# Kernel tuning notes

Hardware: AMD Instinct MI355X
Metric: run time of the kernel (lower is better)

## Reference

```python
import jax, jax.numpy as jnp
import numpy as np

NUM_HEADS = 8

def _qkv(t, W, b, H):
    # t: [B, L, C] -> q, k, v each [B, H, L, D]
    B, L, C = t.shape
    D = C // H
    qkv = (t @ W + b).reshape(B, L, 3, H, D)
    qkv = jnp.moveaxis(qkv, 2, 0)           # [3, B, L, H, D]
    qkv = jnp.swapaxes(qkv, 2, 3)           # [3, B, H, L, D]
    return qkv[0], qkv[1], qkv[2]

def _attend(q, k, v, scale):
    # q,k,v: [B, H, L, D] -> [B, L, C]
    B, H, L, D = q.shape
    scores = jnp.einsum('bhqd,bhkd->bhqk', q, k) * scale
    attn = jax.nn.softmax(scores, axis=-1)
    out = jnp.einsum('bhqk,bhkd->bhqd', attn, v)
    return jnp.swapaxes(out, 1, 2).reshape(B, L, H * D)

def setup_inputs() -> dict:
    key = jax.random.key(0)
    ks = jax.random.split(key, 7)
    B, N, C = 8, 2048, 512
    s_in = 1.0 / np.sqrt(C)
    return {
        'x': jax.random.normal(ks[0], (B, N, C), dtype=jnp.float32),
        'W_rgb_qkv': jax.random.normal(ks[1], (C, 3 * C), dtype=jnp.float32) * s_in,
        'b_rgb_qkv': jax.random.normal(ks[2], (3 * C,), dtype=jnp.float32) * 0.02,
        'W_depth_qkv': jax.random.normal(ks[3], (C, 3 * C), dtype=jnp.float32) * s_in,
        'b_depth_qkv': jax.random.normal(ks[4], (3 * C,), dtype=jnp.float32) * 0.02,
        'W_proj': jax.random.normal(ks[5], (C, C), dtype=jnp.float32) * s_in,
        'b_proj': jax.random.normal(ks[6], (C,), dtype=jnp.float32) * 0.02,
    }

def reference(x, W_rgb_qkv, b_rgb_qkv, W_depth_qkv, b_depth_qkv, W_proj, b_proj):
    B, N, C = x.shape
    H = NUM_HEADS
    D = C // H
    scale = D ** -0.5
    L = N // 2
    rgb, depth = x[:, :L], x[:, L:]
    rq, rk, rv = _qkv(rgb, W_rgb_qkv, b_rgb_qkv, H)
    dq, dk, dv = _qkv(depth, W_depth_qkv, b_depth_qkv, H)
    # rgb queries attend to depth K/V (named depth_v in torch code)
    depth_out = _attend(rq, dk, dv, scale)
    # depth queries attend to rgb K/V (named rgb_v in torch code)
    rgb_out = _attend(dq, rk, rv, scale)
    out = jnp.concatenate([rgb_out, depth_out], axis=1)  # [B, N, C]
    return out @ W_proj + b_proj
```

## Files before the change

### kernel.cpp

```cpp
#include <hip/hip_runtime.h>
#include <hip/hip_bf16.h>

typedef __attribute__((ext_vector_type(8))) short s16x8;
typedef __attribute__((ext_vector_type(4))) float f32x4;

__device__ __forceinline__ ushort f2bf(float f) {
  union { float f; unsigned int u; } c; c.f = f;
  unsigned int u = c.u + 0x7fffu + ((c.u >> 16) & 1u);
  return (ushort)(u >> 16);
}

__device__ __forceinline__ unsigned int pack2(float lo, float hi) {
  __hip_bfloat162 b2 = __float22bfloat162_rn(make_float2(lo, hi));
  union { __hip_bfloat162 b; unsigned int u; } c; c.b = b2;
  return c.u;
}

__device__ __forceinline__ s16x8 ld16(const ushort* p) {
  union { uint4 u; s16x8 s; } c;
  c.u = *reinterpret_cast<const uint4*>(p);
  return c.s;
}

__device__ __forceinline__ f32x4 mfma16(s16x8 a, s16x8 b, f32x4 c) {
  return __builtin_amdgcn_mfma_f32_16x16x32_bf16(a, b, c, 0, 0, 0);
}

__device__ __forceinline__ float exp2fast(float x) { return __builtin_amdgcn_exp2f(x); }

__device__ __forceinline__ void gld_lds16(const void* g, void* l) {
  __builtin_amdgcn_global_load_lds(
      (const __attribute__((address_space(1))) void*)g,
      (__attribute__((address_space(3))) void*)l, 16, 0, 0);
}


__global__ __launch_bounds__(256) void k_prep(
    const float* __restrict__ x, ushort* __restrict__ xb,
    const float* __restrict__ Wr, ushort* __restrict__ WtR,
    const float* __restrict__ Wd, ushort* __restrict__ WtD,
    const float* __restrict__ Wp, ushort* __restrict__ WtP) {
  __shared__ float tile[32][33];
  int b = blockIdx.x, t = threadIdx.x;
  if (b < 8192) {
    int i = (b * 256 + t) * 4;
    float4 v = *reinterpret_cast<const float4*>(x + i);
    ushort4 o;
    o.x = f2bf(v.x); o.y = f2bf(v.y); o.z = f2bf(v.z); o.w = f2bf(v.w);
    *reinterpret_cast<ushort4*>(xb + i) = o;
    return;
  }
  b -= 8192;
  const float* src; ushort* dst; int N;
  if (b < 768)      { src = Wr; dst = WtR; N = 1536; }
  else if (b < 1536){ b -= 768;  src = Wd; dst = WtD; N = 1536; }
  else              { b -= 1536; src = Wp; dst = WtP; N = 512; }
  int nb = N >> 5;
  int n0 = (b % nb) * 32, k0 = (b / nb) * 32;
  int tx = t & 31, ty = t >> 5;
#pragma unroll
  for (int i = 0; i < 32; i += 8)
    tile[ty + i][tx] = src[(k0 + ty + i) * N + (n0 + tx)];
  __syncthreads();
#pragma unroll
  for (int i = 0; i < 32; i += 8)
    dst[(size_t)(n0 + ty + i) * 512 + (k0 + tx)] = f2bf(tile[tx][ty + i]);
}


__device__ __forceinline__ void stage_lds(const ushort* __restrict__ src, int ld,
                                          char* ldsbase, int t) {
#pragma unroll
  for (int p = 0; p < 4; ++p) {
    int chunk = p * 256 + t;
    int r = chunk >> 3, cc = chunk & 7;
    gld_lds16(src + r * ld + ((cc ^ (r & 7)) * 8), ldsbase + (chunk & ~63) * 16);
  }
}

__device__ __forceinline__ s16x8 lds_frag(const char* lds, int row, int c) {
  union { uint4 u; s16x8 s; } cv;
  cv.u = *reinterpret_cast<const uint4*>(lds + row * 128 + ((c ^ (row & 7)) * 16));
  return cv.s;
}


template <bool TRANS>
__global__ __launch_bounds__(256) void k_qkv(
    const ushort* __restrict__ xb, const ushort* __restrict__ WtR,
    const ushort* __restrict__ WtD, const float* __restrict__ bR,
    const float* __restrict__ bD, ushort* __restrict__ Qb,
    ushort* __restrict__ Kb, ushort* __restrict__ Vt) {
  __shared__ __align__(16) char lds[65536];
  int m0 = blockIdx.x * 128;
  int n0 = (TRANS ? 1024 : 0) + blockIdx.y * 128;
  int s = m0 >> 13, bb = (m0 >> 10) & 7, lbase = m0 & 1023;
  const ushort* A = xb + (size_t)(bb * 2048 + s * 1024 + lbase) * 512;
  const ushort* Wt = (s ? WtD : WtR) + (size_t)n0 * 512;
  const float* bias = s ? bD : bR;
  int t = threadIdx.x;
  int wid = t >> 6, ln = t & 15, g = (t & 63) >> 4;
  int wr = wid >> 1, wc = wid & 1;
  f32x4 acc[4][4] = {};
  stage_lds(A, 512, lds, t);
  stage_lds(Wt, 512, lds + 16384, t);
  __syncthreads();
  for (int ks = 0; ks < 8; ++ks) {
    char* cbuf = lds + (ks & 1) * 32768;
    if (ks < 7) {
      char* nbuf = lds + ((ks + 1) & 1) * 32768;
      stage_lds(A + (ks + 1) * 64, 512, nbuf, t);
      stage_lds(Wt + (ks + 1) * 64, 512, nbuf + 16384, t);
    }
    char* ldsA = cbuf;
    char* ldsB = cbuf + 16384;
#pragma unroll
    for (int kk = 0; kk < 2; ++kk) {
      s16x8 af[4], bf[4];
#pragma unroll
      for (int mi = 0; mi < 4; ++mi) af[mi] = lds_frag(ldsA, wr * 64 + mi * 16 + ln, kk * 4 + g);
#pragma unroll
      for (int ni = 0; ni < 4; ++ni) bf[ni] = lds_frag(ldsB, wc * 64 + ni * 16 + ln, kk * 4 + g);
#pragma unroll
      for (int mi = 0; mi < 4; ++mi)
#pragma unroll
        for (int ni = 0; ni < 4; ++ni)
          acc[mi][ni] = TRANS ? mfma16(bf[ni], af[mi], acc[mi][ni])
                              : mfma16(af[mi], bf[ni], acc[mi][ni]);
    }
    __syncthreads();
  }
  int hb_base = (s * 8 + bb) * 8;
  if (!TRANS) {
    bool isK = (n0 >> 9) != 0;
    ushort* dst = isK ? Kb : Qb;
    float sc = isK ? 1.0f : 0.18033688011112042f;
#pragma unroll
    for (int mi = 0; mi < 4; ++mi)
#pragma unroll
      for (int ni = 0; ni < 4; ++ni) {
        f32x4 v = acc[mi][ni];
        int col = n0 + wc * 64 + ni * 16 + ln;
        int h = (col >> 6) & 7, d = col & 63;
        float bv = bias[col];
        ushort* hp = dst + ((size_t)(hb_base + h) << 16);
        int lr = lbase + wr * 64 + mi * 16 + g * 4;
#pragma unroll
        for (int j = 0; j < 4; ++j) hp[(lr + j) * 64 + d] = f2bf((v[j] + bv) * sc);
      }
  } else {
#pragma unroll
    for (int mi = 0; mi < 4; ++mi)
#pragma unroll
      for (int ni = 0; ni < 4; ++ni) {
        f32x4 v = acc[mi][ni];
        int nb = n0 + wc * 64 + ni * 16 + g * 4;
        int mm = m0 + wr * 64 + mi * 16 + ln;
        int l = mm & 1023;
        int lp = (l & ~63) | (l & 0x23) | ((l & 0x0C) << 1) | ((l & 0x10) >> 2);
#pragma unroll
        for (int j = 0; j < 4; ++j) {
          int col = nb + j;
          int h = (col >> 6) & 7, d = col & 63;
          Vt[((size_t)(hb_base + h) << 16) + d * 1024 + lp] = f2bf(v[j] + bias[col]);
        }
      }
  }
}


__global__ __launch_bounds__(512) void k_attn(const ushort* __restrict__ Qb,
                                              const ushort* __restrict__ Kb,
                                              const ushort* __restrict__ Vt,
                                              ushort* __restrict__ AO) {
  __shared__ __align__(16) char lds[32768];
  int bid = blockIdx.x;
  int set = bid & 127, qb = bid >> 7;
  int pair = set & 1, h = (set >> 1) & 7, bb = set >> 4;
  int sQ = 1 - pair, sKV = pair;
  const ushort* Qp = Qb + ((size_t)((sQ * 8 + bb) * 8 + h) << 16);
  const ushort* Kp = Kb + ((size_t)((sKV * 8 + bb) * 8 + h) << 16);
  const ushort* Vp = Vt + ((size_t)((sKV * 8 + bb) * 8 + h) << 16);
  int t = threadIdx.x, w = t >> 6, ln = t & 15, g = (t & 63) >> 4;
  int q0 = qb * 256 + w * 32;
  s16x8 qf0a = ld16(Qp + (q0 + ln) * 64 + g * 8);
  s16x8 qf1a = ld16(Qp + (q0 + ln) * 64 + 32 + g * 8);
  s16x8 qf0b = ld16(Qp + (q0 + 16 + ln) * 64 + g * 8);
  s16x8 qf1b = ld16(Qp + (q0 + 16 + ln) * 64 + 32 + g * 8);

  int r = t >> 3, cc = t & 7;
  int kof = r * 64 + ((cc ^ (r & 7)) * 8);
  int vof = r * 1024 + ((cc ^ (r & 7)) * 8);
  int ldst = (t & ~63) * 16;

  float ls_a = 0.f, ls_b = 0.f;
  f32x4 oca[4] = {}, ocb[4] = {};

  const ushort* kstage = Kp;
  const ushort* vstage = Vp;

  char* kc = lds;
  char* vc = lds + 8192;
  char* kn = lds + 16384;
  char* vn = lds + 24576;

  gld_lds16(kstage + kof, kc + ldst);
  gld_lds16(vstage + vof, vc + ldst);
  kstage += 4096; vstage += 64;
  asm volatile("s_waitcnt vmcnt(0)" ::: "memory");
  __builtin_amdgcn_sched_barrier(0);
  __builtin_amdgcn_s_barrier();
  __builtin_amdgcn_sched_barrier(0);

  for (int it = 0; it < 16; ++it) {
    if (it < 15) {
      gld_lds16(kstage + kof, kn + ldst);
      gld_lds16(vstage + vof, vn + ldst);
      kstage += 4096; vstage += 64;
    }

    f32x4 za[4], zb[4];
    __builtin_amdgcn_s_setprio(1);
#pragma unroll
    for (int s = 0; s < 4; ++s) {
      s16x8 k0 = lds_frag(kc, s * 16 + ln, g);
      s16x8 k1 = lds_frag(kc, s * 16 + ln, 4 + g);
      f32x4 z1 = {}; z1 = mfma16(k0, qf0a, z1); z1 = mfma16(k1, qf1a, z1); za[s] = z1;
      f32x4 z2 = {}; z2 = mfma16(k0, qf0b, z2); z2 = mfma16(k1, qf1b, z2); zb[s] = z2;
    }
    __builtin_amdgcn_s_setprio(0);

    unsigned int pwa[8], pwb[8];
#pragma unroll
    for (int s = 0; s < 4; ++s) {
      float p0 = exp2fast(za[s][0]), p1 = exp2fast(za[s][1]);
      float p2 = exp2fast(za[s][2]), p3 = exp2fast(za[s][3]);
      ls_a += (p0 + p1) + (p2 + p3);
      pwa[2 * s] = pack2(p0, p1); pwa[2 * s + 1] = pack2(p2, p3);
      float r0 = exp2fast(zb[s][0]), r1 = exp2fast(zb[s][1]);
      float r2 = exp2fast(zb[s][2]), r3 = exp2fast(zb[s][3]);
      ls_b += (r0 + r1) + (r2 + r3);
      pwb[2 * s] = pack2(r0, r1); pwb[2 * s + 1] = pack2(r2, r3);
    }
    union { uint4 u; s16x8 v; } c0, c1, c2, c3;
    c0.u = make_uint4(pwa[0], pwa[1], pwa[2], pwa[3]);
    c1.u = make_uint4(pwa[4], pwa[5], pwa[6], pwa[7]);
    c2.u = make_uint4(pwb[0], pwb[1], pwb[2], pwb[3]);
    c3.u = make_uint4(pwb[4], pwb[5], pwb[6], pwb[7]);
    s16x8 pf0a = c0.v, pf1a = c1.v, pf0b = c2.v, pf1b = c3.v;

    __builtin_amdgcn_s_setprio(1);
#pragma unroll
    for (int d = 0; d < 4; ++d) {
      s16x8 v0 = lds_frag(vc, d * 16 + ln, g);
      s16x8 v1 = lds_frag(vc, d * 16 + ln, 4 + g);
      oca[d] = mfma16(v0, pf0a, oca[d]);
      oca[d] = mfma16(v1, pf1a, oca[d]);
      ocb[d] = mfma16(v0, pf0b, ocb[d]);
      ocb[d] = mfma16(v1, pf1b, ocb[d]);
    }
    __builtin_amdgcn_s_setprio(0);

    if (it < 15) {
      asm volatile("s_waitcnt vmcnt(0)" ::: "memory");
      __builtin_amdgcn_sched_barrier(0);
      __builtin_amdgcn_s_barrier();
      __builtin_amdgcn_sched_barrier(0);
    }
    char* tk = kc; kc = kn; kn = tk;
    char* tv = vc; vc = vn; vn = tv;
  }

  ls_a += __shfl_xor(ls_a, 16, 64);
  ls_a += __shfl_xor(ls_a, 32, 64);
  ls_b += __shfl_xor(ls_b, 16, 64);
  ls_b += __shfl_xor(ls_b, 32, 64);
  float inva = 1.0f / ls_a, invb = 1.0f / ls_b;
  int orow = bb * 2048 + pair * 1024 + q0 + ln;
#pragma unroll
  for (int d = 0; d < 4; ++d) {
    uint2 st;
    st.x = pack2(oca[d][0] * inva, oca[d][1] * inva);
    st.y = pack2(oca[d][2] * inva, oca[d][3] * inva);
    *reinterpret_cast<uint2*>(AO + (size_t)orow * 512 + h * 64 + d * 16 + 4 * g) = st;
    uint2 st2;
    st2.x = pack2(ocb[d][0] * invb, ocb[d][1] * invb);
    st2.y = pack2(ocb[d][2] * invb, ocb[d][3] * invb);
    *reinterpret_cast<uint2*>(AO + (size_t)(orow + 16) * 512 + h * 64 + d * 16 + 4 * g) = st2;
  }
}


__global__ __launch_bounds__(256) void k_gemm_proj(const ushort* __restrict__ AO,
                                                   const ushort* __restrict__ WtP,
                                                   const float* __restrict__ bP,
                                                   float* __restrict__ Out) {
  __shared__ __align__(16) char lds[65536];
  int m0 = blockIdx.x * 128, n0 = blockIdx.y * 128;
  const ushort* A = AO + (size_t)m0 * 512;
  const ushort* Wt = WtP + (size_t)n0 * 512;
  int t = threadIdx.x;
  int wid = t >> 6, ln = t & 15, g = (t & 63) >> 4;
  int wr = wid >> 1, wc = wid & 1;
  f32x4 acc[4][4] = {};
  stage_lds(A, 512, lds, t);
  stage_lds(Wt, 512, lds + 16384, t);
  __syncthreads();
  for (int ks = 0; ks < 8; ++ks) {
    char* cbuf = lds + (ks & 1) * 32768;
    if (ks < 7) {
      char* nbuf = lds + ((ks + 1) & 1) * 32768;
      stage_lds(A + (ks + 1) * 64, 512, nbuf, t);
      stage_lds(Wt + (ks + 1) * 64, 512, nbuf + 16384, t);
    }
    char* ldsA = cbuf;
    char* ldsB = cbuf + 16384;
#pragma unroll
    for (int kk = 0; kk < 2; ++kk) {
      s16x8 af[4], bf[4];
#pragma unroll
      for (int mi = 0; mi < 4; ++mi) af[mi] = lds_frag(ldsA, wr * 64 + mi * 16 + ln, kk * 4 + g);
#pragma unroll
      for (int ni = 0; ni < 4; ++ni) bf[ni] = lds_frag(ldsB, wc * 64 + ni * 16 + ln, kk * 4 + g);
#pragma unroll
      for (int mi = 0; mi < 4; ++mi)
#pragma unroll
        for (int ni = 0; ni < 4; ++ni) acc[mi][ni] = mfma16(af[mi], bf[ni], acc[mi][ni]);
    }
    __syncthreads();
  }
#pragma unroll
  for (int mi = 0; mi < 4; ++mi)
#pragma unroll
    for (int ni = 0; ni < 4; ++ni) {
      f32x4 v = acc[mi][ni];
      int col = n0 + wc * 64 + ni * 16 + ln;
      float bv = bP[col];
      int r0 = m0 + wr * 64 + mi * 16 + g * 4;
#pragma unroll
      for (int j = 0; j < 4; ++j) Out[(size_t)(r0 + j) * 512 + col] = v[j] + bv;
    }
}


extern "C" void kernel_launch(void* const* d_in, const int* in_sizes, int n_in,
                              void* d_out, int out_size, void* d_ws, size_t ws_size,
                              hipStream_t stream) {
  const float* x      = (const float*)d_in[0];
  const float* W_rgb  = (const float*)d_in[1];
  const float* b_rgb  = (const float*)d_in[2];
  const float* W_dep  = (const float*)d_in[3];
  const float* b_dep  = (const float*)d_in[4];
  const float* W_proj = (const float*)d_in[5];
  const float* b_proj = (const float*)d_in[6];
  float* out = (float*)d_out;

  char* ws = (char*)d_ws;
  ushort* xb  = (ushort*)(ws + 0);
  ushort* WtR = (ushort*)(ws + 16777216);
  ushort* WtD = (ushort*)(ws + 18350080);
  ushort* WtP = (ushort*)(ws + 19922944);
  ushort* Qb  = (ushort*)(ws + 20447232);
  ushort* Kb  = (ushort*)(ws + 37224448);
  ushort* Vt  = (ushort*)(ws + 54001664);
  ushort* AO  = (ushort*)(ws + 70778880);

  k_prep<<<9984, 256, 0, stream>>>(x, xb, W_rgb, WtR, W_dep, WtD, W_proj, WtP);
  k_qkv<false><<<dim3(128, 8), 256, 0, stream>>>(xb, WtR, WtD, b_rgb, b_dep, Qb, Kb, Vt);
  k_qkv<true><<<dim3(128, 4), 256, 0, stream>>>(xb, WtR, WtD, b_rgb, b_dep, Qb, Kb, Vt);
  k_attn<<<512, 512, 0, stream>>>(Qb, Kb, Vt, AO);
  k_gemm_proj<<<dim3(128, 4), 256, 0, stream>>>(AO, WtP, b_proj, out);
}
```

Baseline: 137.1 us.

## Triple-buffer K/V loads in attention and stage V-transpose stores through LDS

```diff
diff --git a/kernel.cpp b/kernel.cpp
--- a/kernel.cpp
+++ b/kernel.cpp
@@ -149,22 +149,36 @@
         for (int j = 0; j < 4; ++j) hp[(lr + j) * 64 + d] = f2bf((v[j] + bv) * sc);
       }
   } else {
-#pragma unroll
-    for (int mi = 0; mi < 4; ++mi)
+    ushort* et = (ushort*)lds;
+#pragma unroll
+    for (int mi = 0; mi < 4; ++mi) {
+      int ll = wr * 64 + mi * 16 + ln;
+      int lpl = (ll & ~63) | (ll & 0x23) | ((ll & 0x0C) << 1) | ((ll & 0x10) >> 2);
+      int chunk = lpl >> 3, within = lpl & 7;
 #pragma unroll
       for (int ni = 0; ni < 4; ++ni) {
         f32x4 v = acc[mi][ni];
-        int nb = n0 + wc * 64 + ni * 16 + g * 4;
-        int mm = m0 + wr * 64 + mi * 16 + ln;
-        int l = mm & 1023;
-        int lp = (l & ~63) | (l & 0x23) | ((l & 0x0C) << 1) | ((l & 0x10) >> 2);
+        int crb = wc * 64 + ni * 16 + g * 4;
 #pragma unroll
         for (int j = 0; j < 4; ++j) {
-          int col = nb + j;
-          int h = (col >> 6) & 7, d = col & 63;
-          Vt[((size_t)(hb_base + h) << 16) + d * 1024 + lp] = f2bf(v[j] + bias[col]);
+          int cr = crb + j;
+          float bv = bias[n0 + cr];
+          *(ushort*)((char*)et + cr * 256 + ((chunk ^ (cr & 15)) * 16) + within * 2)
+              = f2bf(v[j] + bv);
         }
       }
+    }
+    __syncthreads();
+#pragma unroll
+    for (int pass = 0; pass < 8; ++pass) {
+      int rrow = pass * 16 + (t >> 4);
+      int c16 = t & 15;
+      int col = n0 + rrow;
+      int h = (col >> 6) & 7, d = col & 63;
+      uint4 vv = *(const uint4*)((const char*)et + rrow * 256 + ((c16 ^ (rrow & 15)) * 16));
+      *reinterpret_cast<uint4*>(Vt + ((size_t)(hb_base + h) << 16) + d * 1024 + lbase + c16 * 8)
+          = vv;
+    }
   }
 }
 
@@ -173,7 +187,7 @@
                                               const ushort* __restrict__ Kb,
                                               const ushort* __restrict__ Vt,
                                               ushort* __restrict__ AO) {
-  __shared__ __align__(16) char lds[32768];
+  __shared__ __align__(16) char lds[49152];
   int bid = blockIdx.x;
   int set = bid & 127, qb = bid >> 7;
   int pair = set & 1, h = (set >> 1) & 7, bb = set >> 4;
@@ -199,23 +213,25 @@
   const ushort* kstage = Kp;
   const ushort* vstage = Vp;
 
-  char* kc = lds;
-  char* vc = lds + 8192;
-  char* kn = lds + 16384;
-  char* vn = lds + 24576;
-
-  gld_lds16(kstage + kof, kc + ldst);
-  gld_lds16(vstage + vof, vc + ldst);
+  char* bc = lds;
+  char* bn = lds + 16384;
+  char* bs = lds + 32768;
+
+  gld_lds16(kstage + kof, bc + ldst);
+  gld_lds16(vstage + vof, bc + 8192 + ldst);
   kstage += 4096; vstage += 64;
-  asm volatile("s_waitcnt vmcnt(0)" ::: "memory");
+  gld_lds16(kstage + kof, bn + ldst);
+  gld_lds16(vstage + vof, bn + 8192 + ldst);
+  kstage += 4096; vstage += 64;
+  asm volatile("s_waitcnt vmcnt(2)" ::: "memory");
   __builtin_amdgcn_sched_barrier(0);
   __builtin_amdgcn_s_barrier();
   __builtin_amdgcn_sched_barrier(0);
 
   for (int it = 0; it < 16; ++it) {
-    if (it < 15) {
-      gld_lds16(kstage + kof, kn + ldst);
-      gld_lds16(vstage + vof, vn + ldst);
+    if (it < 14) {
+      gld_lds16(kstage + kof, bs + ldst);
+      gld_lds16(vstage + vof, bs + 8192 + ldst);
       kstage += 4096; vstage += 64;
     }
 
@@ -223,8 +239,8 @@
     __builtin_amdgcn_s_setprio(1);
 #pragma unroll
     for (int s = 0; s < 4; ++s) {
-      s16x8 k0 = lds_frag(kc, s * 16 + ln, g);
-      s16x8 k1 = lds_frag(kc, s * 16 + ln, 4 + g);
+      s16x8 k0 = lds_frag(bc, s * 16 + ln, g);
+      s16x8 k1 = lds_frag(bc, s * 16 + ln, 4 + g);
       f32x4 z1 = {}; z1 = mfma16(k0, qf0a, z1); z1 = mfma16(k1, qf1a, z1); za[s] = z1;
       f32x4 z2 = {}; z2 = mfma16(k0, qf0b, z2); z2 = mfma16(k1, qf1b, z2); zb[s] = z2;
     }
@@ -252,8 +268,8 @@
     __builtin_amdgcn_s_setprio(1);
 #pragma unroll
     for (int d = 0; d < 4; ++d) {
-      s16x8 v0 = lds_frag(vc, d * 16 + ln, g);
-      s16x8 v1 = lds_frag(vc, d * 16 + ln, 4 + g);
+      s16x8 v0 = lds_frag(bc + 8192, d * 16 + ln, g);
+      s16x8 v1 = lds_frag(bc + 8192, d * 16 + ln, 4 + g);
       oca[d] = mfma16(v0, pf0a, oca[d]);
       oca[d] = mfma16(v1, pf1a, oca[d]);
       ocb[d] = mfma16(v0, pf0b, ocb[d]);
@@ -262,13 +278,16 @@
     __builtin_amdgcn_s_setprio(0);
 
     if (it < 15) {
-      asm volatile("s_waitcnt vmcnt(0)" ::: "memory");
+      if (it < 14) {
+        asm volatile("s_waitcnt vmcnt(2)" ::: "memory");
+      } else {
+        asm volatile("s_waitcnt vmcnt(0)" ::: "memory");
+      }
       __builtin_amdgcn_sched_barrier(0);
       __builtin_amdgcn_s_barrier();
       __builtin_amdgcn_sched_barrier(0);
     }
-    char* tk = kc; kc = kn; kn = tk;
-    char* tv = vc; vc = vn; vn = tv;
+    char* tmp = bc; bc = bn; bn = bs; bs = tmp;
   }
 
   ls_a += __shfl_xor(ls_a, 16, 64);
```

Measured after the change: 137.8 us. Within noise of the previous version (+0.5%).
